# Performance work log

Measured on AMD Instinct MI355X. Metric: run time of the kernel, lower is better.

## Reference

```python
import jax, jax.numpy as jnp
import numpy as np

N_ATOMS = 100_000
N_BONDS = 200_000
MAX_NB = 6
HIDDEN = 300
ATOM_FD = 133
BOND_FD = 147
DEPTH = 3
ATOMS_PER_MOL = 20
N_MOLS = N_ATOMS // ATOMS_PER_MOL


def setup_inputs() -> dict:
    key = jax.random.key(0)
    ks = jax.random.split(key, 9)
    f_atoms = jax.random.normal(ks[0], (N_ATOMS, ATOM_FD), dtype=jnp.float32)
    f_bonds = jax.random.normal(ks[1], (N_BONDS, BOND_FD), dtype=jnp.float32)
    a2b = jax.random.randint(ks[2], (N_ATOMS, MAX_NB), 0, N_BONDS, dtype=jnp.int32)
    b2a = jax.random.randint(ks[3], (N_BONDS,), 0, N_ATOMS, dtype=jnp.int32)
    b2revb = jax.random.randint(ks[4], (N_BONDS,), 0, N_BONDS, dtype=jnp.int32)
    mol_ids = (jnp.arange(N_ATOMS, dtype=jnp.int32) // ATOMS_PER_MOL).astype(jnp.int32)
    W_i = jax.random.normal(ks[5], (BOND_FD, HIDDEN), dtype=jnp.float32) * 0.05
    W_h = jax.random.normal(ks[6], (HIDDEN, HIDDEN), dtype=jnp.float32) * 0.05
    W_o = jax.random.normal(ks[7], (ATOM_FD + HIDDEN, HIDDEN), dtype=jnp.float32) * 0.05
    b_o = jax.random.normal(ks[8], (HIDDEN,), dtype=jnp.float32) * 0.05
    return {"f_atoms": f_atoms, "f_bonds": f_bonds, "a2b": a2b, "b2a": b2a,
            "b2revb": b2revb, "mol_ids": mol_ids, "W_i": W_i, "W_h": W_h,
            "W_o": W_o, "b_o": b_o}


def reference(f_atoms, f_bonds, a2b, b2a, b2revb, mol_ids, W_i, W_h, W_o, b_o):
    # input = W_i(f_bonds); message = act(input)
    inp = f_bonds @ W_i                     # [n_bonds, H]
    message = jax.nn.relu(inp)
    for _ in range(DEPTH - 1):
        # padded-neighbor gather + sum over incoming bonds per atom
        a_message = message[a2b].sum(axis=1)          # [n_atoms, H]
        # forward gather minus reverse-bond message
        m = a_message[b2a] - message[b2revb]          # [n_bonds, H]
        message = jax.nn.relu(inp + m @ W_h)          # (dropout p=0 omitted)
    # final atom readout
    a_message = message[a2b].sum(axis=1)              # [n_atoms, H]
    a_input = jnp.concatenate([f_atoms, a_message], axis=1)  # [n_atoms, atom_fd+H]
    atom_hiddens = jax.nn.relu(a_input @ W_o + b_o)   # [n_atoms, H]
    # 'mean' pooling over each molecule's atoms (contiguous equal-size scopes)
    mol_sums = jax.ops.segment_sum(atom_hiddens, mol_ids, num_segments=N_MOLS)
    return mol_sums / ATOMS_PER_MOL                   # [n_mols, H]
```

## Files before the change

### kernel.cpp

```cpp
#include <hip/hip_runtime.h>
#include <hip/hip_bf16.h>
#include <hip/hip_fp8.h>

#define N_ATOMS 100000
#define N_BONDS 200000
#define MAX_NB 6
#define HIDDEN 300
#define HP 320
#define CH 40
#define ATOM_FD 133
#define BOND_FD 147
#define N_MOLS 5000
#define APM 20

#define NT32 10
#define KKI32 10
#define KKH32 20
#define KKO32 28

using bf16 = __hip_bfloat16;
typedef __attribute__((ext_vector_type(8))) short short8v;
typedef __attribute__((ext_vector_type(4))) float float4v;
typedef __attribute__((ext_vector_type(2))) float float2v;
typedef __attribute__((ext_vector_type(16))) float float16v;
typedef unsigned int u32;
typedef unsigned short u16;
typedef unsigned char u8;

__device__ __forceinline__ float us2f(u16 u) {
    union { u32 i; float f; } v; v.i = ((u32)u) << 16; return v.f;
}
__device__ __forceinline__ u16 f2us(float f) {
    bf16 h = __float2bfloat16(f);
    return *(u16*)&h;
}
__device__ __forceinline__ u32 pack2(float a, float b) {
    return (u32)f2us(a) | ((u32)f2us(b) << 16);
}
__device__ __forceinline__ uint2 pack4(const float4v& a) {
    uint2 o; o.x = pack2(a[0], a[1]); o.y = pack2(a[2], a[3]); return o;
}

#if defined(__has_builtin)
#if __has_builtin(__builtin_amdgcn_cvt_f32_fp8) && __has_builtin(__builtin_amdgcn_cvt_pk_fp8_f32)
#define HW_FP8 1
#endif
#if __has_builtin(__builtin_amdgcn_cvt_pk_f32_fp8)
#define HW_FP8_PK 1
#endif
#endif

__device__ __forceinline__ void f8x4_to_f32(u32 p, float* o) {
#if defined(HW_FP8_PK)
    float2v lo = __builtin_amdgcn_cvt_pk_f32_fp8(p, false);
    float2v hi = __builtin_amdgcn_cvt_pk_f32_fp8(p, true);
    o[0] = lo[0]; o[1] = lo[1]; o[2] = hi[0]; o[3] = hi[1];
#elif defined(HW_FP8)
    o[0] = __builtin_amdgcn_cvt_f32_fp8(p, 0);
    o[1] = __builtin_amdgcn_cvt_f32_fp8(p, 1);
    o[2] = __builtin_amdgcn_cvt_f32_fp8(p, 2);
    o[3] = __builtin_amdgcn_cvt_f32_fp8(p, 3);
#else
#pragma unroll
    for (int i = 0; i < 4; ++i) {
        __hip_fp8_e4m3 h; h.__x = (u8)(p >> (8 * i));
        o[i] = (float)h;
    }
#endif
}
__device__ __forceinline__ u32 f32x4_to_f8(float a, float b, float c, float d) {
#ifdef HW_FP8
    u32 r = __builtin_amdgcn_cvt_pk_fp8_f32(a, b, 0u, false);
    r = __builtin_amdgcn_cvt_pk_fp8_f32(c, d, r, true);
    return r;
#else
    __hip_fp8_e4m3 ha(a), hb(b), hc(c), hd(d);
    return (u32)ha.__x | ((u32)hb.__x << 8) | ((u32)hc.__x << 16) | ((u32)hd.__x << 24);
#endif
}
__device__ __forceinline__ void f8x16_to_f32(uint4 u, float* o) {
    f8x4_to_f32(u.x, o); f8x4_to_f32(u.y, o + 4);
    f8x4_to_f32(u.z, o + 8); f8x4_to_f32(u.w, o + 12);
}
__device__ __forceinline__ u32 relu_f8x4(u32 u) {
    u32 m = (u >> 7) & 0x01010101u;
    return u & ~(m * 255u);
}
__device__ __forceinline__ uint4 relu_f8x16(uint4 u) {
    u.x = relu_f8x4(u.x); u.y = relu_f8x4(u.y);
    u.z = relu_f8x4(u.z); u.w = relu_f8x4(u.w);
    return u;
}

__global__ __launch_bounds__(64) void pack_w32(const float* __restrict__ src,
                                               short* __restrict__ dst,
                                               int Ksrc, int mode) {
    int kk = blockIdx.x / NT32, nt = blockIdx.x % NT32;
    int lane = threadIdx.x;
    int col = nt * 32 + (lane & 31);
#pragma unroll
    for (int j = 0; j < 8; ++j) {
        int k = kk * 16 + (lane >> 5) * 8 + j;
        float v = 0.f;
        if (k < Ksrc && col < HIDDEN) {
            int krow = k;
            if (mode == 2) krow = (k < HIDDEN) ? (ATOM_FD + k) : (k - HIDDEN);
            v = src[krow * HIDDEN + col];
        }
        dst[(((kk * NT32 + nt) << 6) + lane) * 8 + j] = (short)f2us(v);
    }
}

__global__ __launch_bounds__(320) void k1_input(const float* __restrict__ fb,
                                                const short8v* __restrict__ WiP,
                                                u8* __restrict__ inp8) {
    __shared__ __align__(16) char sm[32 * 640];
    const int tid = threadIdx.x;
    const long base = (long)blockIdx.x * 32;
    const float4* src4 = (const float4*)(fb + base * BOND_FD);
#pragma unroll
    for (int it = 0; it < 4; ++it) {
        int idx = tid + it * 320;
        if (idx < 1176) {
            float4 v = src4[idx];
            int f = idx * 4;
#pragma unroll
            for (int e = 0; e < 4; ++e) {
                int g = f + e;
                int r = g / BOND_FD, c = g - r * BOND_FD;
                int byte = r * 320 + c * 2;
                *(u16*)(sm + (byte ^ ((r & 7) << 4))) = f2us(((const float*)&v)[e]);
            }
        }
    }
    for (int i = tid; i < 32 * 13; i += 320) {
        int r = i / 13, c = BOND_FD + i % 13;
        int byte = r * 320 + c * 2;
        *(u16*)(sm + (byte ^ ((r & 7) << 4))) = 0;
    }
    __syncthreads();

    const int lane = tid & 63, wave = tid >> 6;
    const int row = lane & 31, hi = lane >> 5;
    const int nt0 = wave * 2;
    float16v acc0, acc1;
#pragma unroll
    for (int q = 0; q < 16; ++q) { acc0[q] = 0.f; acc1[q] = 0.f; }
    for (int kk = 0; kk < KKI32; ++kk) {
        int byte = row * 320 + kk * 32 + hi * 16;
        short8v a = *(const short8v*)(sm + (byte ^ ((row & 7) << 4)));
        short8v w0 = WiP[((kk * NT32 + nt0) << 6) + lane];
        short8v w1 = WiP[((kk * NT32 + nt0 + 1) << 6) + lane];
        acc0 = __builtin_amdgcn_mfma_f32_32x32x16_bf16(w0, a, acc0, 0, 0, 0);
        acc1 = __builtin_amdgcn_mfma_f32_32x32x16_bf16(w1, a, acc1, 0, 0, 0);
    }
    __syncthreads();
#pragma unroll
    for (int t = 0; t < 2; ++t) {
#pragma unroll
        for (int q = 0; q < 4; ++q) {
            int colb = (nt0 + t) * 32 + q * 8 + hi * 4;
            float a0 = (t == 0 ? acc0[4 * q + 0] : acc1[4 * q + 0]);
            float a1 = (t == 0 ? acc0[4 * q + 1] : acc1[4 * q + 1]);
            float a2 = (t == 0 ? acc0[4 * q + 2] : acc1[4 * q + 2]);
            float a3 = (t == 0 ? acc0[4 * q + 3] : acc1[4 * q + 3]);
            *(u32*)(sm + row * 336 + colb) = f32x4_to_f8(a0, a1, a2, a3);
        }
    }
    __syncthreads();
#pragma unroll
    for (int it = 0; it < 2; ++it) {
        int i = tid + it * 320;
        int r = i / 20, c = i % 20;
        uint4 v = *(const uint4*)(sm + r * 336 + c * 16);
        ((uint4*)(inp8 + (base + r) * 320))[c] = v;
    }
}

template<int RELU>
__global__ __launch_bounds__(256, 8) void k2_gather(const u8* __restrict__ src,
                                                    const int* __restrict__ a2b,
                                                    u8* __restrict__ dst) {
    int id = blockIdx.x * 256 + threadIdx.x;
    int atom = id / 10, c2 = id % 10;
    if (atom >= N_ATOMS) return;
    const int* nb = a2b + atom * MAX_NB;
    float s[32];
#pragma unroll
    for (int q = 0; q < 32; ++q) s[q] = 0.f;
#pragma unroll
    for (int j = 0; j < MAX_NB; ++j) {
        const uint4* rp = (const uint4*)(src + (long)nb[j] * 320);
        uint4 u0 = rp[2 * c2];
        uint4 u1 = rp[2 * c2 + 1];
        if (RELU) { u0 = relu_f8x16(u0); u1 = relu_f8x16(u1); }
        float v[16];
        f8x16_to_f32(u0, v);
#pragma unroll
        for (int q = 0; q < 16; ++q) s[q] += v[q];
        f8x16_to_f32(u1, v);
#pragma unroll
        for (int q = 0; q < 16; ++q) s[16 + q] += v[q];
    }
    uint4 o0, o1;
    o0.x = f32x4_to_f8(s[0], s[1], s[2], s[3]);
    o0.y = f32x4_to_f8(s[4], s[5], s[6], s[7]);
    o0.z = f32x4_to_f8(s[8], s[9], s[10], s[11]);
    o0.w = f32x4_to_f8(s[12], s[13], s[14], s[15]);
    o1.x = f32x4_to_f8(s[16], s[17], s[18], s[19]);
    o1.y = f32x4_to_f8(s[20], s[21], s[22], s[23]);
    o1.z = f32x4_to_f8(s[24], s[25], s[26], s[27]);
    o1.w = f32x4_to_f8(s[28], s[29], s[30], s[31]);
    uint4* dp = (uint4*)(dst + (long)atom * 320);
    dp[2 * c2] = o0;
    dp[2 * c2 + 1] = o1;
}

template<int RELUSRC>
__global__ __launch_bounds__(320) void kzf_update(const u8* __restrict__ inp8,
                                                  const u8* __restrict__ AM,
                                                  const u8* __restrict__ msgsrc,
                                                  const int* __restrict__ b2a,
                                                  const int* __restrict__ b2revb,
                                                  const short8v* __restrict__ WhP,
                                                  u8* __restrict__ msgdst) {
    __shared__ __align__(16) char sm[32 * 640];
    const int tid = threadIdx.x;
    const long base = (long)blockIdx.x * 32;

#pragma unroll
    for (int it = 0; it < 2; ++it) {
        int i = tid + it * 320;
        int r = i / 20, c = i % 20;
        long b = base + r;
        int ia = b2a[b], ir = b2revb[b];
        uint4 ua = ((const uint4*)(AM + (long)ia * 320))[c];
        uint4 um = ((const uint4*)(msgsrc + (long)ir * 320))[c];
        if (RELUSRC) um = relu_f8x16(um);
        float av[16], mv[16];
        f8x16_to_f32(ua, av);
        f8x16_to_f32(um, mv);
        uint4 o0, o1;
        o0.x = pack2(av[0] - mv[0], av[1] - mv[1]);
        o0.y = pack2(av[2] - mv[2], av[3] - mv[3]);
        o0.z = pack2(av[4] - mv[4], av[5] - mv[5]);
        o0.w = pack2(av[6] - mv[6], av[7] - mv[7]);
        o1.x = pack2(av[8] - mv[8], av[9] - mv[9]);
        o1.y = pack2(av[10] - mv[10], av[11] - mv[11]);
        o1.z = pack2(av[12] - mv[12], av[13] - mv[13]);
        o1.w = pack2(av[14] - mv[14], av[15] - mv[15]);
        int byte = r * 640 + c * 32;
        int swz = (r & 7) << 4;
        *(uint4*)(sm + (byte ^ swz)) = o0;
        *(uint4*)(sm + ((byte + 16) ^ swz)) = o1;
    }
    __syncthreads();

    const int lane = tid & 63, wave = tid >> 6;
    const int row = lane & 31, hi = lane >> 5;
    const int nt0 = wave * 2;
    float16v acc0, acc1;
#pragma unroll
    for (int q = 0; q < 16; ++q) { acc0[q] = 0.f; acc1[q] = 0.f; }
    for (int kk = 0; kk < KKH32; ++kk) {
        int byte = row * 640 + kk * 32 + hi * 16;
        short8v a = *(const short8v*)(sm + (byte ^ ((row & 7) << 4)));
        short8v w0 = WhP[((kk * NT32 + nt0) << 6) + lane];
        short8v w1 = WhP[((kk * NT32 + nt0 + 1) << 6) + lane];
        acc0 = __builtin_amdgcn_mfma_f32_32x32x16_bf16(w0, a, acc0, 0, 0, 0);
        acc1 = __builtin_amdgcn_mfma_f32_32x32x16_bf16(w1, a, acc1, 0, 0, 0);
    }
    __syncthreads();
#pragma unroll
    for (int t = 0; t < 2; ++t) {
#pragma unroll
        for (int q = 0; q < 4; ++q) {
            int colb = (nt0 + t) * 32 + q * 8 + hi * 4;
            u32 u = *(const u32*)(inp8 + (base + row) * 320 + colb);
            float iv[4];
            f8x4_to_f32(u, iv);
            float a0 = (t == 0 ? acc0[4 * q + 0] : acc1[4 * q + 0]);
            float a1 = (t == 0 ? acc0[4 * q + 1] : acc1[4 * q + 1]);
            float a2 = (t == 0 ? acc0[4 * q + 2] : acc1[4 * q + 2]);
            float a3 = (t == 0 ? acc0[4 * q + 3] : acc1[4 * q + 3]);
            float v0 = fmaxf(a0 + iv[0], 0.f);
            float v1 = fmaxf(a1 + iv[1], 0.f);
            float v2 = fmaxf(a2 + iv[2], 0.f);
            float v3 = fmaxf(a3 + iv[3], 0.f);
            *(u32*)(sm + row * 336 + colb) = f32x4_to_f8(v0, v1, v2, v3);
        }
    }
    __syncthreads();
#pragma unroll
    for (int it = 0; it < 2; ++it) {
        int i = tid + it * 320;
        int r = i / 20, c = i % 20;
        uint4 v = *(const uint4*)(sm + r * 336 + c * 16);
        ((uint4*)(msgdst + (base + r) * 320))[c] = v;
    }
}

__global__ __launch_bounds__(320) void k4_gemm(const float* __restrict__ fa,
                                               const u8* __restrict__ msg,
                                               const int* __restrict__ a2b,
                                               const short8v* __restrict__ WoP,
                                               const float* __restrict__ bo,
                                               u16* __restrict__ ah) {
    __shared__ __align__(16) char sm[32 * 896];
    const int tid = threadIdx.x;
    const long base = (long)blockIdx.x * 32;
#pragma unroll
    for (int it = 0; it < 2; ++it) {
        int i = tid + it * 320;
        if (i < 608) {
            int row = i / 19, c = i % 19;
            long atom = base + row;
            const int* nb = a2b + atom * MAX_NB;
            float s[16];
#pragma unroll
            for (int q = 0; q < 16; ++q) s[q] = 0.f;
#pragma unroll
            for (int j = 0; j < MAX_NB; ++j) {
                uint4 u = ((const uint4*)(msg + (long)nb[j] * 320))[c];
                float v[16];
                f8x16_to_f32(u, v);
#pragma unroll
                for (int q = 0; q < 16; ++q) s[q] += v[q];
            }
            uint4 o0, o1;
            o0.x = pack2(s[0], s[1]);  o0.y = pack2(s[2], s[3]);
            o0.z = pack2(s[4], s[5]);  o0.w = pack2(s[6], s[7]);
            o1.x = pack2(s[8], s[9]);  o1.y = pack2(s[10], s[11]);
            o1.z = pack2(s[12], s[13]); o1.w = pack2(s[14], s[15]);
            int byte = row * 896 + c * 32;
            int swz = (row & 7) << 4;
            *(uint4*)(sm + (byte ^ swz)) = o0;
            if (c < 18) {
                *(uint4*)(sm + ((byte + 16) ^ swz)) = o1;
            } else {
                *(uint2*)(sm + ((byte + 16) ^ swz)) = make_uint2(o1.x, o1.y);
            }
        }
    }
    const float4* src4 = (const float4*)(fa + base * ATOM_FD);
#pragma unroll
    for (int it = 0; it < 4; ++it) {
        int idx = tid + it * 320;
        if (idx < 1064) {
            float4 v = src4[idx];
            int f = idx * 4;
#pragma unroll
            for (int e = 0; e < 4; ++e) {
                int g = f + e;
                int r = g / ATOM_FD, c2 = g - r * ATOM_FD;
                int byte = r * 896 + (HIDDEN + c2) * 2;
                *(u16*)(sm + (byte ^ ((r & 7) << 4))) = f2us(((const float*)&v)[e]);
            }
        }
    }
    for (int i = tid; i < 480; i += 320) {
        int r = i / 15, c2 = ATOM_FD + i % 15;
        int byte = r * 896 + (HIDDEN + c2) * 2;
        *(u16*)(sm + (byte ^ ((r & 7) << 4))) = 0;
    }
    __syncthreads();

    const int lane = tid & 63, wave = tid >> 6;
    const int row = lane & 31, hi = lane >> 5;
    const int nt0 = wave * 2;
    float16v acc0, acc1;
#pragma unroll
    for (int q = 0; q < 16; ++q) { acc0[q] = 0.f; acc1[q] = 0.f; }
    for (int kk = 0; kk < KKO32; ++kk) {
        int byte = row * 896 + kk * 32 + hi * 16;
        short8v a = *(const short8v*)(sm + (byte ^ ((row & 7) << 4)));
        short8v w0 = WoP[((kk * NT32 + nt0) << 6) + lane];
        short8v w1 = WoP[((kk * NT32 + nt0 + 1) << 6) + lane];
        acc0 = __builtin_amdgcn_mfma_f32_32x32x16_bf16(w0, a, acc0, 0, 0, 0);
        acc1 = __builtin_amdgcn_mfma_f32_32x32x16_bf16(w1, a, acc1, 0, 0, 0);
    }
    __syncthreads();
#pragma unroll
    for (int t = 0; t < 2; ++t) {
#pragma unroll
        for (int q = 0; q < 4; ++q) {
            int colb = (nt0 + t) * 32 + q * 8 + hi * 4;
            float4v v;
#pragma unroll
            for (int d = 0; d < 4; ++d) {
                float bias = (colb + d < HIDDEN) ? bo[colb + d] : 0.f;
                float av = (t == 0 ? acc0[4 * q + d] : acc1[4 * q + d]);
                v[d] = fmaxf(av + bias, 0.f);
            }
            int byte = row * 640 + colb * 2;
            *(uint2*)(sm + (byte ^ ((row & 7) << 4))) = pack4(v);
        }
    }
    __syncthreads();
#pragma unroll
    for (int it = 0; it < 4; ++it) {
        int i = tid + it * 320;
        int r = i / CH, c = i % CH;
        int byte = r * 640 + c * 16;
        uint4 v = *(const uint4*)(sm + (byte ^ ((r & 7) << 4)));
        ((uint4*)(ah + (base + r) * HP))[c] = v;
    }
}

__global__ __launch_bounds__(320) void k5_pool(const u16* __restrict__ ah,
                                               float* __restrict__ out) {
    const int h = threadIdx.x;
    const int mol = blockIdx.x;
    if (h >= HIDDEN) return;
    float s = 0.f;
#pragma unroll
    for (int a = 0; a < APM; ++a)
        s += us2f(ah[((long)mol * APM + a) * HP + h]);
    out[(long)mol * HIDDEN + h] = s * (1.f / APM);
}

extern "C" void kernel_launch(void* const* d_in, const int* in_sizes, int n_in,
                              void* d_out, int out_size, void* d_ws, size_t ws_size,
                              hipStream_t stream) {
    const float* f_atoms = (const float*)d_in[0];
    const float* f_bonds = (const float*)d_in[1];
    const int* a2b = (const int*)d_in[2];
    const int* b2a = (const int*)d_in[3];
    const int* b2revb = (const int*)d_in[4];
    const float* Wi = (const float*)d_in[6];
    const float* Wh = (const float*)d_in[7];
    const float* Wo = (const float*)d_in[8];
    const float* bo = (const float*)d_in[9];
    float* out = (float*)d_out;

    char* ws = (char*)d_ws;
    size_t off = 0;
    auto alloc = [&](size_t bytes) {
        void* p = ws + off;
        off = (off + bytes + 255) & ~(size_t)255;
        return p;
    };
    u8* inp8  = (u8*)alloc((size_t)N_BONDS * 320);
    u8* msgA  = (u8*)alloc((size_t)N_BONDS * 320);
    u8* msgB  = (u8*)alloc((size_t)N_BONDS * 320);
    u8* AM    = (u8*)alloc((size_t)N_ATOMS * 320);
    short* WiP32 = (short*)alloc((size_t)KKI32 * NT32 * 64 * 8 * sizeof(short));
    short* WhP32 = (short*)alloc((size_t)KKH32 * NT32 * 64 * 8 * sizeof(short));
    short* WoP32 = (short*)alloc((size_t)KKO32 * NT32 * 64 * 8 * sizeof(short));
    u16* ah = (u16*)msgA;

    pack_w32<<<KKI32 * NT32, 64, 0, stream>>>(Wi, WiP32, BOND_FD, 0);
    pack_w32<<<KKH32 * NT32, 64, 0, stream>>>(Wh, WhP32, HIDDEN, 0);
    pack_w32<<<KKO32 * NT32, 64, 0, stream>>>(Wo, WoP32, ATOM_FD + HIDDEN, 2);

    k1_input<<<N_BONDS / 32, 320, 0, stream>>>(f_bonds, (const short8v*)WiP32, inp8);

    const int g2 = (N_ATOMS * 10 + 255) / 256;
    k2_gather<1><<<g2, 256, 0, stream>>>(inp8, a2b, AM);
    kzf_update<1><<<N_BONDS / 32, 320, 0, stream>>>(inp8, AM, inp8, b2a, b2revb,
                                                    (const short8v*)WhP32, msgA);
    k2_gather<0><<<g2, 256, 0, stream>>>(msgA, a2b, AM);
    kzf_update<0><<<N_BONDS / 32, 320, 0, stream>>>(inp8, AM, msgA, b2a, b2revb,
                                                    (const short8v*)WhP32, msgB);
    k4_gemm<<<N_ATOMS / 32, 320, 0, stream>>>(f_atoms, msgB, a2b,
                                              (const short8v*)WoP32, bo, ah);
    k5_pool<<<N_MOLS, 320, 0, stream>>>(ah, out);
}
```

Baseline: 449.4 us.

## Fuse mean pooling into readout GEMM with atomics; batch gather loads

```diff
diff --git a/kernel.cpp b/kernel.cpp
--- a/kernel.cpp
+++ b/kernel.cpp
@@ -109,6 +109,11 @@
         }
         dst[(((kk * NT32 + nt) << 6) + lane) * 8 + j] = (short)f2us(v);
     }
+}
+
+__global__ __launch_bounds__(256) void k0_zero(float* __restrict__ out) {
+    int i = blockIdx.x * 256 + threadIdx.x;
+    if (i < N_MOLS * HIDDEN) out[i] = 0.f;
 }
 
 __global__ __launch_bounds__(320) void k1_input(const float* __restrict__ fb,
@@ -228,31 +233,38 @@
     const int tid = threadIdx.x;
     const long base = (long)blockIdx.x * 32;
 
-#pragma unroll
-    for (int it = 0; it < 2; ++it) {
-        int i = tid + it * 320;
-        int r = i / 20, c = i % 20;
-        long b = base + r;
-        int ia = b2a[b], ir = b2revb[b];
-        uint4 ua = ((const uint4*)(AM + (long)ia * 320))[c];
-        uint4 um = ((const uint4*)(msgsrc + (long)ir * 320))[c];
-        if (RELUSRC) um = relu_f8x16(um);
-        float av[16], mv[16];
-        f8x16_to_f32(ua, av);
-        f8x16_to_f32(um, mv);
-        uint4 o0, o1;
-        o0.x = pack2(av[0] - mv[0], av[1] - mv[1]);
-        o0.y = pack2(av[2] - mv[2], av[3] - mv[3]);
-        o0.z = pack2(av[4] - mv[4], av[5] - mv[5]);
-        o0.w = pack2(av[6] - mv[6], av[7] - mv[7]);
-        o1.x = pack2(av[8] - mv[8], av[9] - mv[9]);
-        o1.y = pack2(av[10] - mv[10], av[11] - mv[11]);
-        o1.z = pack2(av[12] - mv[12], av[13] - mv[13]);
-        o1.w = pack2(av[14] - mv[14], av[15] - mv[15]);
-        int byte = r * 640 + c * 32;
-        int swz = (r & 7) << 4;
-        *(uint4*)(sm + (byte ^ swz)) = o0;
-        *(uint4*)(sm + ((byte + 16) ^ swz)) = o1;
+    {
+        const int r0 = tid / 20, c0 = tid % 20;
+        const int i1 = tid + 320;
+        const int r1 = i1 / 20, c1 = i1 % 20;
+        int ia0 = b2a[base + r0], ir0 = b2revb[base + r0];
+        int ia1 = b2a[base + r1], ir1 = b2revb[base + r1];
+        uint4 ua0 = ((const uint4*)(AM + (long)ia0 * 320))[c0];
+        uint4 um0 = ((const uint4*)(msgsrc + (long)ir0 * 320))[c0];
+        uint4 ua1 = ((const uint4*)(AM + (long)ia1 * 320))[c1];
+        uint4 um1 = ((const uint4*)(msgsrc + (long)ir1 * 320))[c1];
+        if (RELUSRC) { um0 = relu_f8x16(um0); um1 = relu_f8x16(um1); }
+#pragma unroll
+        for (int t = 0; t < 2; ++t) {
+            uint4 ua = t ? ua1 : ua0, um = t ? um1 : um0;
+            int r = t ? r1 : r0, c = t ? c1 : c0;
+            float av[16], mv[16];
+            f8x16_to_f32(ua, av);
+            f8x16_to_f32(um, mv);
+            uint4 o0, o1;
+            o0.x = pack2(av[0] - mv[0], av[1] - mv[1]);
+            o0.y = pack2(av[2] - mv[2], av[3] - mv[3]);
+            o0.z = pack2(av[4] - mv[4], av[5] - mv[5]);
+            o0.w = pack2(av[6] - mv[6], av[7] - mv[7]);
+            o1.x = pack2(av[8] - mv[8], av[9] - mv[9]);
+            o1.y = pack2(av[10] - mv[10], av[11] - mv[11]);
+            o1.z = pack2(av[12] - mv[12], av[13] - mv[13]);
+            o1.w = pack2(av[14] - mv[14], av[15] - mv[15]);
+            int byte = r * 640 + c * 32;
+            int swz = (r & 7) << 4;
+            *(uint4*)(sm + (byte ^ swz)) = o0;
+            *(uint4*)(sm + ((byte + 16) ^ swz)) = o1;
+        }
     }
     __syncthreads();
 
@@ -305,7 +317,7 @@
                                                const int* __restrict__ a2b,
                                                const short8v* __restrict__ WoP,
                                                const float* __restrict__ bo,
-                                               u16* __restrict__ ah) {
+                                               float* __restrict__ out) {
     __shared__ __align__(16) char sm[32 * 896];
     const int tid = threadIdx.x;
     const long base = (long)blockIdx.x * 32;
@@ -316,17 +328,31 @@
             int row = i / 19, c = i % 19;
             long atom = base + row;
             const int* nb = a2b + atom * MAX_NB;
-            float s[16];
-#pragma unroll
-            for (int q = 0; q < 16; ++q) s[q] = 0.f;
-#pragma unroll
-            for (int j = 0; j < MAX_NB; ++j) {
-                uint4 u = ((const uint4*)(msg + (long)nb[j] * 320))[c];
-                float v[16];
-                f8x16_to_f32(u, v);
-#pragma unroll
-                for (int q = 0; q < 16; ++q) s[q] += v[q];
-            }
+            int n0 = nb[0], n1 = nb[1], n2 = nb[2];
+            int n3 = nb[3], n4 = nb[4], n5 = nb[5];
+            uint4 u0 = ((const uint4*)(msg + (long)n0 * 320))[c];
+            uint4 u1 = ((const uint4*)(msg + (long)n1 * 320))[c];
+            uint4 u2 = ((const uint4*)(msg + (long)n2 * 320))[c];
+            uint4 u3 = ((const uint4*)(msg + (long)n3 * 320))[c];
+            uint4 u4 = ((const uint4*)(msg + (long)n4 * 320))[c];
+            uint4 u5 = ((const uint4*)(msg + (long)n5 * 320))[c];
+            float s[16], v[16];
+            f8x16_to_f32(u0, s);
+            f8x16_to_f32(u1, v);
+#pragma unroll
+            for (int q = 0; q < 16; ++q) s[q] += v[q];
+            f8x16_to_f32(u2, v);
+#pragma unroll
+            for (int q = 0; q < 16; ++q) s[q] += v[q];
+            f8x16_to_f32(u3, v);
+#pragma unroll
+            for (int q = 0; q < 16; ++q) s[q] += v[q];
+            f8x16_to_f32(u4, v);
+#pragma unroll
+            for (int q = 0; q < 16; ++q) s[q] += v[q];
+            f8x16_to_f32(u5, v);
+#pragma unroll
+            for (int q = 0; q < 16; ++q) s[q] += v[q];
             uint4 o0, o1;
             o0.x = pack2(s[0], s[1]);  o0.y = pack2(s[2], s[3]);
             o0.z = pack2(s[4], s[5]);  o0.w = pack2(s[6], s[7]);
@@ -397,26 +423,22 @@
         }
     }
     __syncthreads();
-#pragma unroll
-    for (int it = 0; it < 4; ++it) {
-        int i = tid + it * 320;
-        int r = i / CH, c = i % CH;
-        int byte = r * 640 + c * 16;
-        uint4 v = *(const uint4*)(sm + (byte ^ ((r & 7) << 4)));
-        ((uint4*)(ah + (base + r) * HP))[c] = v;
-    }
-}
-
-__global__ __launch_bounds__(320) void k5_pool(const u16* __restrict__ ah,
-                                               float* __restrict__ out) {
-    const int h = threadIdx.x;
-    const int mol = blockIdx.x;
-    if (h >= HIDDEN) return;
-    float s = 0.f;
-#pragma unroll
-    for (int a = 0; a < APM; ++a)
-        s += us2f(ah[((long)mol * APM + a) * HP + h]);
-    out[(long)mol * HIDDEN + h] = s * (1.f / APM);
+    const int mfirst = (int)(base / APM);
+    const int mlast = (int)((base + 31) / APM);
+    const int nseg = mlast - mfirst + 1;
+    for (int idx = tid; idx < nseg * HIDDEN; idx += 320) {
+        int s = idx / HIDDEN, col = idx % HIDDEN;
+        int m = mfirst + s;
+        long a0 = (long)m * APM; if (a0 < base) a0 = base;
+        long a1 = (long)(m + 1) * APM; if (a1 > base + 32) a1 = base + 32;
+        float sum = 0.f;
+        for (long a = a0; a < a1; ++a) {
+            int r = (int)(a - base);
+            int byte = r * 640 + col * 2;
+            sum += us2f(*(const u16*)(sm + (byte ^ ((r & 7) << 4))));
+        }
+        atomicAdd(out + (long)m * HIDDEN + col, sum * (1.f / APM));
+    }
 }
 
 extern "C" void kernel_launch(void* const* d_in, const int* in_sizes, int n_in,
@@ -447,11 +469,11 @@
     short* WiP32 = (short*)alloc((size_t)KKI32 * NT32 * 64 * 8 * sizeof(short));
     short* WhP32 = (short*)alloc((size_t)KKH32 * NT32 * 64 * 8 * sizeof(short));
     short* WoP32 = (short*)alloc((size_t)KKO32 * NT32 * 64 * 8 * sizeof(short));
-    u16* ah = (u16*)msgA;
 
     pack_w32<<<KKI32 * NT32, 64, 0, stream>>>(Wi, WiP32, BOND_FD, 0);
     pack_w32<<<KKH32 * NT32, 64, 0, stream>>>(Wh, WhP32, HIDDEN, 0);
     pack_w32<<<KKO32 * NT32, 64, 0, stream>>>(Wo, WoP32, ATOM_FD + HIDDEN, 2);
+    k0_zero<<<(N_MOLS * HIDDEN + 255) / 256, 256, 0, stream>>>(out);
 
     k1_input<<<N_BONDS / 32, 320, 0, stream>>>(f_bonds, (const short8v*)WiP32, inp8);
 
@@ -463,6 +485,5 @@
     kzf_update<0><<<N_BONDS / 32, 320, 0, stream>>>(inp8, AM, msgA, b2a, b2revb,
                                                     (const short8v*)WhP32, msgB);
     k4_gemm<<<N_ATOMS / 32, 320, 0, stream>>>(f_atoms, msgB, a2b,
-                                              (const short8v*)WoP32, bo, ah);
-    k5_pool<<<N_MOLS, 320, 0, stream>>>(ah, out);
-}
+                                              (const short8v*)WoP32, bo, out);
+}
```

Result: faster. 439.0 us (-2.3%).

## Fuse mean pooling into readout GEMM via atomics and reuse gather kernel

Applied to the files above, without the earlier changes.

```diff
diff --git a/kernel.cpp b/kernel.cpp
--- a/kernel.cpp
+++ b/kernel.cpp
@@ -109,6 +109,11 @@
         }
         dst[(((kk * NT32 + nt) << 6) + lane) * 8 + j] = (short)f2us(v);
     }
+}
+
+__global__ __launch_bounds__(256) void k0_zero(float* __restrict__ out) {
+    int i = blockIdx.x * 256 + threadIdx.x;
+    if (i < N_MOLS * HIDDEN) out[i] = 0.f;
 }
 
 __global__ __launch_bounds__(320) void k1_input(const float* __restrict__ fb,
@@ -301,11 +306,10 @@
 }
 
 __global__ __launch_bounds__(320) void k4_gemm(const float* __restrict__ fa,
-                                               const u8* __restrict__ msg,
-                                               const int* __restrict__ a2b,
+                                               const u8* __restrict__ AM,
                                                const short8v* __restrict__ WoP,
                                                const float* __restrict__ bo,
-                                               u16* __restrict__ ah) {
+                                               float* __restrict__ out) {
     __shared__ __align__(16) char sm[32 * 896];
     const int tid = threadIdx.x;
     const long base = (long)blockIdx.x * 32;
@@ -314,19 +318,9 @@
         int i = tid + it * 320;
         if (i < 608) {
             int row = i / 19, c = i % 19;
-            long atom = base + row;
-            const int* nb = a2b + atom * MAX_NB;
+            uint4 u = ((const uint4*)(AM + (base + row) * 320))[c];
             float s[16];
-#pragma unroll
-            for (int q = 0; q < 16; ++q) s[q] = 0.f;
-#pragma unroll
-            for (int j = 0; j < MAX_NB; ++j) {
-                uint4 u = ((const uint4*)(msg + (long)nb[j] * 320))[c];
-                float v[16];
-                f8x16_to_f32(u, v);
-#pragma unroll
-                for (int q = 0; q < 16; ++q) s[q] += v[q];
-            }
+            f8x16_to_f32(u, s);
             uint4 o0, o1;
             o0.x = pack2(s[0], s[1]);  o0.y = pack2(s[2], s[3]);
             o0.z = pack2(s[4], s[5]);  o0.w = pack2(s[6], s[7]);
@@ -397,26 +391,22 @@
         }
     }
     __syncthreads();
-#pragma unroll
-    for (int it = 0; it < 4; ++it) {
-        int i = tid + it * 320;
-        int r = i / CH, c = i % CH;
-        int byte = r * 640 + c * 16;
-        uint4 v = *(const uint4*)(sm + (byte ^ ((r & 7) << 4)));
-        ((uint4*)(ah + (base + r) * HP))[c] = v;
-    }
-}
-
-__global__ __launch_bounds__(320) void k5_pool(const u16* __restrict__ ah,
-                                               float* __restrict__ out) {
-    const int h = threadIdx.x;
-    const int mol = blockIdx.x;
-    if (h >= HIDDEN) return;
-    float s = 0.f;
-#pragma unroll
-    for (int a = 0; a < APM; ++a)
-        s += us2f(ah[((long)mol * APM + a) * HP + h]);
-    out[(long)mol * HIDDEN + h] = s * (1.f / APM);
+    const int mfirst = (int)(base / APM);
+    const int mlast = (int)((base + 31) / APM);
+    const int nseg = mlast - mfirst + 1;
+    for (int idx = tid; idx < nseg * HIDDEN; idx += 320) {
+        int s = idx / HIDDEN, col = idx % HIDDEN;
+        int m = mfirst + s;
+        long a0 = (long)m * APM; if (a0 < base) a0 = base;
+        long a1 = (long)(m + 1) * APM; if (a1 > base + 32) a1 = base + 32;
+        float sum = 0.f;
+        for (long a = a0; a < a1; ++a) {
+            int r = (int)(a - base);
+            int byte = r * 640 + col * 2;
+            sum += us2f(*(const u16*)(sm + (byte ^ ((r & 7) << 4))));
+        }
+        atomicAdd(out + (long)m * HIDDEN + col, sum * (1.f / APM));
+    }
 }
 
 extern "C" void kernel_launch(void* const* d_in, const int* in_sizes, int n_in,
@@ -447,11 +437,11 @@
     short* WiP32 = (short*)alloc((size_t)KKI32 * NT32 * 64 * 8 * sizeof(short));
     short* WhP32 = (short*)alloc((size_t)KKH32 * NT32 * 64 * 8 * sizeof(short));
     short* WoP32 = (short*)alloc((size_t)KKO32 * NT32 * 64 * 8 * sizeof(short));
-    u16* ah = (u16*)msgA;
 
     pack_w32<<<KKI32 * NT32, 64, 0, stream>>>(Wi, WiP32, BOND_FD, 0);
     pack_w32<<<KKH32 * NT32, 64, 0, stream>>>(Wh, WhP32, HIDDEN, 0);
     pack_w32<<<KKO32 * NT32, 64, 0, stream>>>(Wo, WoP32, ATOM_FD + HIDDEN, 2);
+    k0_zero<<<(N_MOLS * HIDDEN + 255) / 256, 256, 0, stream>>>(out);
 
     k1_input<<<N_BONDS / 32, 320, 0, stream>>>(f_bonds, (const short8v*)WiP32, inp8);
 
@@ -462,7 +452,7 @@
     k2_gather<0><<<g2, 256, 0, stream>>>(msgA, a2b, AM);
     kzf_update<0><<<N_BONDS / 32, 320, 0, stream>>>(inp8, AM, msgA, b2a, b2revb,
                                                     (const short8v*)WhP32, msgB);
-    k4_gemm<<<N_ATOMS / 32, 320, 0, stream>>>(f_atoms, msgB, a2b,
-                                              (const short8v*)WoP32, bo, ah);
-    k5_pool<<<N_MOLS, 320, 0, stream>>>(ah, out);
-}
+    k2_gather<0><<<g2, 256, 0, stream>>>(msgB, a2b, AM);
+    k4_gemm<<<N_ATOMS / 32, 320, 0, stream>>>(f_atoms, AM,
+                                              (const short8v*)WoP32, bo, out);
+}
```

Measured after the change: 448.4 us. Within noise of the previous version (-0.2%).
